# Performance work log

Hardware: AMD Instinct MI355X
Metric: run time of the kernel (lower is better)

Reference implementation:

```python
import jax, jax.numpy as jnp
import numpy as np

N_HEADS = 8
EMBED_C = 256  # key/query channels
OUT_C = 256    # value/output channels
MASK_CENTER = True

def setup_inputs() -> dict:
    key = jax.random.key(0)
    ks = jax.random.split(key, 5)
    B, C, H, W = 32, 256, 32, 32
    x = jax.random.normal(ks[0], (B, C, H, W), dtype=jnp.float32)
    # 1x1 conv weights as [out, in] matrices; scaled like torch conv default init
    s = 1.0 / np.sqrt(C)
    q_w = jax.random.normal(ks[1], (EMBED_C, C), dtype=jnp.float32) * s
    q_b = jax.random.normal(ks[2], (EMBED_C,), dtype=jnp.float32) * s
    kv_w = jax.random.normal(ks[3], (EMBED_C + OUT_C, C), dtype=jnp.float32) * s
    kv_b = jax.random.normal(ks[4], (EMBED_C + OUT_C,), dtype=jnp.float32) * s
    return {"x": x, "q_w": q_w, "q_b": q_b, "kv_w": kv_w, "kv_b": kv_b}

def _to_multihead(t):
    # t: (B, C, S) -> (B, n_heads, S, C // n_heads)
    B, C, S = t.shape
    return jnp.transpose(t.reshape(B, N_HEADS, C // N_HEADS, S), (0, 1, 3, 2))

def reference(x, q_w, q_b, kv_w, kv_b):
    B, C, H, W = x.shape
    S = H * W
    xf = x.reshape(B, C, S)  # flatten spatial; 1x1 conv == channel matmul
    q = jnp.einsum('oc,bcs->bos', q_w, xf) + q_b[None, :, None]
    kv = jnp.einsum('oc,bcs->bos', kv_w, xf) + kv_b[None, :, None]
    k, v = kv[:, :EMBED_C], kv[:, EMBED_C:]
    q = _to_multihead(q)   # (B, h, S, dk)
    k = _to_multihead(k)   # (B, h, S, dk)
    v = _to_multihead(v)   # (B, h, S, dv)
    dk = k.shape[-1]
    # strictly-lower-triangular causal mask (center pixel masked)
    mask = jnp.tril(jnp.ones((S, S), dtype=x.dtype), -int(MASK_CENTER))
    scores = jnp.einsum('bhqd,bhkd->bhqk', q, k) / jnp.sqrt(jnp.asarray(dk, x.dtype))
    scores = jnp.where(mask == 0, jnp.asarray(-10000.0, x.dtype), scores)
    attn = jax.nn.softmax(scores, axis=-1)
    attn = jnp.where(mask == 0, jnp.asarray(0.0, x.dtype), attn)
    out = jnp.einsum('bhqk,bhkd->bhqd', attn, v)  # (B, h, S, dv)
    out = jnp.transpose(out, (0, 1, 3, 2)).reshape(B, OUT_C, H, W)
    return out
```

## Files before the change

kernel.cpp:

```cpp
#include <hip/hip_runtime.h>
#include <hip/hip_bf16.h>

typedef __attribute__((ext_vector_type(8))) short short8;
typedef __attribute__((ext_vector_type(4))) float f32x4;
typedef __attribute__((ext_vector_type(16))) float f32x16;

#define B_  32
#define CH  256
#define S_  1024
#define NH  8
#define HD  32

static __device__ __forceinline__ unsigned short f2bf(float f) {
  __hip_bfloat16 h = __float2bfloat16(f);
  return *reinterpret_cast<unsigned short*>(&h);
}

static __device__ __forceinline__ void gl_lds16(const void* g, void* l) {
  __builtin_amdgcn_global_load_lds(
      (const __attribute__((address_space(1))) void*)g,
      (__attribute__((address_space(3))) void*)l, 16, 0, 0);
}

__global__ void k_prep(const float* __restrict__ x, unsigned short* __restrict__ xt,
                       const float* __restrict__ qw, const float* __restrict__ qb,
                       const float* __restrict__ kvw, const float* __restrict__ kvb,
                       unsigned short* __restrict__ wt, float* __restrict__ bias) {
  __shared__ float tile[32][33];
  int blk = (int)blockIdx.x;
  int t = threadIdx.x;
  if (blk < 8192) {
    int b = blk >> 8;
    int inner = blk & 255;
    int ct = inner >> 5, st = inner & 31;
    int c0 = ct * 32, s0 = st * 32;
    int r = t >> 3, q4 = (t & 7) * 4;
    const float4 v = *reinterpret_cast<const float4*>(
        x + ((size_t)(b * CH + c0 + r)) * S_ + s0 + q4);
    tile[r][q4 + 0] = v.x; tile[r][q4 + 1] = v.y;
    tile[r][q4 + 2] = v.z; tile[r][q4 + 3] = v.w;
    __syncthreads();
    ushort4 u;
    u.x = f2bf(tile[q4 + 0][r]); u.y = f2bf(tile[q4 + 1][r]);
    u.z = f2bf(tile[q4 + 2][r]); u.w = f2bf(tile[q4 + 3][r]);
    *reinterpret_cast<ushort4*>(xt + ((size_t)(b * S_ + s0 + r)) * CH + c0 + q4) = u;
  } else {
    int gid = (blk - 8192) * 256 + t;
    const float rs = 0.25503531838951954f;
    int o = gid >> 8, c = gid & 255;
    float v = (o < 256) ? qw[o * 256 + c] * rs : kvw[(o - 256) * 256 + c];
    wt[gid] = f2bf(v);
    if (gid < 768) bias[gid] = (gid < 256) ? qb[gid] * rs : kvb[gid - 256];
  }
}

__global__ __launch_bounds__(256) void k_proj(
    const unsigned short* __restrict__ wt, const float* __restrict__ bias,
    const unsigned short* __restrict__ xt,
    unsigned short* __restrict__ qws, unsigned short* __restrict__ kv) {
  __shared__ __align__(16) unsigned short As[2][4096];
  __shared__ __align__(16) unsigned short Bs[2][4096];
  int b = blockIdx.y;
  int mt = blockIdx.x >> 3, nt = blockIdx.x & 7;
  int tid = threadIdx.x;
  int wid = tid >> 6, l = tid & 63;
  int rb = l >> 4, lr = l & 15;
  int wr = wid >> 1, wc = wid & 1;
  int mb = mt * 128, nb = nt * 128;
  int wm = wr * 64, wn = wc * 64;
  const unsigned short* xb = xt + (size_t)b * S_ * CH;

  int r0 = tid >> 2, k0 = (tid & 3) * 8;
  int r1 = (tid + 256) >> 2, k1 = ((tid + 256) & 3) * 8;
  const unsigned short* wa0 = wt + (size_t)(mb + r0) * CH + k0;
  const unsigned short* wa1 = wt + (size_t)(mb + r1) * CH + k1;
  const unsigned short* xb0 = xb + (size_t)(nb + r0) * CH + k0;
  const unsigned short* xb1 = xb + (size_t)(nb + r1) * CH + k1;
  char* asb = (char*)&As[0][0];
  char* bsb = (char*)&Bs[0][0];
  int wb = wid * 1024;

  f32x4 acc[4][4];
  #pragma unroll
  for (int mf = 0; mf < 4; ++mf)
    #pragma unroll
    for (int nf = 0; nf < 4; ++nf)
      acc[mf][nf] = (f32x4){0.f, 0.f, 0.f, 0.f};

  gl_lds16(wa0, asb + wb);
  gl_lds16(wa1, asb + 4096 + wb);
  gl_lds16(xb0, bsb + wb);
  gl_lds16(xb1, bsb + 4096 + wb);
  __syncthreads();

  #pragma unroll 1
  for (int kk = 0; kk < 8; ++kk) {
    int cur = kk & 1;
    bool more = (kk < 7);
    if (more) {
      int ko = (kk + 1) * 32;
      int bo = (cur ^ 1) * 8192 + wb;
      gl_lds16(wa0 + ko, asb + bo);
      gl_lds16(wa1 + ko, asb + 4096 + bo);
      gl_lds16(xb0 + ko, bsb + bo);
      gl_lds16(xb1 + ko, bsb + 4096 + bo);
    }

    short8 a[4], bfr[4];
    #pragma unroll
    for (int mf = 0; mf < 4; ++mf)
      a[mf] = *reinterpret_cast<const short8*>(
          &As[cur][(wm + mf * 16 + lr) * 32 + rb * 8]);
    #pragma unroll
    for (int nf = 0; nf < 4; ++nf)
      bfr[nf] = *reinterpret_cast<const short8*>(
          &Bs[cur][(wn + nf * 16 + lr) * 32 + rb * 8]);
    #pragma unroll
    for (int mf = 0; mf < 4; ++mf)
      #pragma unroll
      for (int nf = 0; nf < 4; ++nf)
        acc[mf][nf] = __builtin_amdgcn_mfma_f32_16x16x32_bf16(
            a[mf], bfr[nf], acc[mf][nf], 0, 0, 0);

    __syncthreads();
  }

  #pragma unroll
  for (int mf = 0; mf < 4; ++mf) {
    int m0 = mb + wm + mf * 16 + rb * 4;
    const float4 bv = *reinterpret_cast<const float4*>(bias + m0);
    #pragma unroll
    for (int nf = 0; nf < 4; ++nf) {
      int n = nb + wn + nf * 16 + lr;
      float v0 = acc[mf][nf][0] + bv.x;
      float v1 = acc[mf][nf][1] + bv.y;
      float v2 = acc[mf][nf][2] + bv.z;
      float v3 = acc[mf][nf][3] + bv.w;
      if (m0 < 256) {
        int h = m0 >> 5, d = m0 & 31;
        ushort4 u = {f2bf(v0), f2bf(v1), f2bf(v2), f2bf(v3)};
        *reinterpret_cast<ushort4*>(
            qws + ((size_t)(b * NH + h) * S_ + n) * HD + d) = u;
      } else if (m0 < 512) {
        int mm = m0 - 256; int h = mm >> 5, d0 = mm & 31;
        size_t off = (((size_t)(b * NH + h) * 32 + (n >> 5)) * 2048)
                   + (size_t)((d0 >> 3) * 256 + (n & 31) * 8 + (d0 & 7));
        ushort4 u = {f2bf(v0), f2bf(v1), f2bf(v2), f2bf(v3)};
        *reinterpret_cast<ushort4*>(kv + off) = u;
      } else {
        int mm = m0 - 512; int h = mm >> 5, d0 = mm & 31;
        int nl = n & 31;
        int kp = (nl & 19) | (((nl >> 2) & 1) << 3) | (((nl >> 3) & 1) << 2);
        size_t base = (((size_t)(b * NH + h) * 32 + (n >> 5)) * 2048) + 1024
                    + (size_t)((kp >> 3) * 256 + (kp & 7));
        kv[base + (size_t)(d0 + 0) * 8] = f2bf(v0);
        kv[base + (size_t)(d0 + 1) * 8] = f2bf(v1);
        kv[base + (size_t)(d0 + 2) * 8] = f2bf(v2);
        kv[base + (size_t)(d0 + 3) * 8] = f2bf(v3);
      }
    }
  }
}

__global__ __launch_bounds__(512, 4) void k_attn(
    const unsigned short* __restrict__ qws, const unsigned short* __restrict__ kv,
    float* __restrict__ out) {
  __shared__ __align__(16) unsigned short kvbuf[2][8192];
  int tid = threadIdx.x;
  int wid = tid >> 6, l = tid & 63;
  int col = l & 31, hi = l >> 5;
  int bh = (int)(blockIdx.x & 255);
  int g  = 3 - (int)(blockIdx.x >> 8);
  int qt = g * 8 + wid;
  int q0 = qt << 5;
  int niter = g * 2 + 2;

  const unsigned short* Q   = qws + (size_t)bh * S_ * HD;
  const unsigned short* kvb = kv + (size_t)bh * 32 * 2048;
  char* kb0 = (char*)&kvbuf[0][0];
  int wb = wid * 1024;

  short8 aq0 = *reinterpret_cast<const short8*>(Q + (q0 + col) * HD + hi * 8);
  short8 aq1 = *reinterpret_cast<const short8*>(Q + (q0 + col) * HD + 16 + hi * 8);

  f32x16 z, O;
  #pragma unroll
  for (int i = 0; i < 16; ++i) { z[i] = 0.f; O[i] = 0.f; }
  float lsA = 0.f, lsB = 0.f;

  gl_lds16(kvb + tid * 8,        kb0 + wb);
  gl_lds16(kvb + 4096 + tid * 8, kb0 + 8192 + wb);
  __syncthreads();

  #pragma unroll 1
  for (int i = 0; i < niter; ++i) {
    int cur = i & 1;
    bool more = (i + 1 < niter);
    if (more) {
      const unsigned short* src = kvb + (size_t)(i + 1) * 8192 + tid * 8;
      char* dst = kb0 + (cur ^ 1) * 16384 + wb;
      gl_lds16(src,        dst);
      gl_lds16(src + 4096, dst + 8192);
    }

    #pragma unroll
    for (int sub = 0; sub < 4; ++sub) {
      int t = 4 * i + sub;
      if (qt >= t) {
        const unsigned short* Kb = &kvbuf[cur][sub * 2048];
        short8 bk0 = *reinterpret_cast<const short8*>(Kb + hi * 256 + col * 8);
        short8 bk1 = *reinterpret_cast<const short8*>(Kb + 512 + hi * 256 + col * 8);
        short8 av0 = *reinterpret_cast<const short8*>(Kb + 1024 + hi * 256 + col * 8);
        short8 av1 = *reinterpret_cast<const short8*>(Kb + 1536 + hi * 256 + col * 8);

        f32x16 st = __builtin_amdgcn_mfma_f32_32x32x16_bf16(bk0, aq0, z, 0, 0, 0);
        st = __builtin_amdgcn_mfma_f32_32x32x16_bf16(bk1, aq1, st, 0, 0, 0);

        float p[16];
        if (t == qt) {
          #pragma unroll
          for (int r = 0; r < 16; ++r) {
            int key = (r & 3) + 8 * (r >> 2) + 4 * hi;
            float e = __builtin_amdgcn_exp2f(st[r]);
            p[r] = (key < col) ? e : 0.f;
          }
        } else {
          #pragma unroll
          for (int r = 0; r < 16; ++r) p[r] = __builtin_amdgcn_exp2f(st[r]);
        }

        lsA += ((p[0] + p[1]) + (p[2] + p[3])) + ((p[4] + p[5]) + (p[6] + p[7]));
        lsB += ((p[8] + p[9]) + (p[10] + p[11])) + ((p[12] + p[13]) + (p[14] + p[15]));

        union { unsigned int u[8]; short8 v[2]; } pb;
        #pragma unroll
        for (int jj = 0; jj < 8; ++jj)
          asm("v_cvt_pk_bf16_f32 %0, %1, %2"
              : "=v"(pb.u[jj]) : "v"(p[2 * jj]), "v"(p[2 * jj + 1]));

        O = __builtin_amdgcn_mfma_f32_32x32x16_bf16(av0, pb.v[0], O, 0, 0, 0);
        O = __builtin_amdgcn_mfma_f32_32x32x16_bf16(av1, pb.v[1], O, 0, 0, 0);
      }
    }

    __syncthreads();
  }

  float lsum = lsA + lsB;
  float ltot = lsum + __shfl_xor(lsum, 32);
  float linv = (ltot > 0.f) ? 1.f / ltot : 0.f;
  int b = bh >> 3, h = bh & 7;
  float* ob = out + ((size_t)(b * 256 + h * 32)) * S_ + q0 + col;
  #pragma unroll
  for (int r = 0; r < 16; ++r) {
    int d = (r & 3) + 8 * (r >> 2) + 4 * hi;
    ob[(size_t)d * S_] = O[r] * linv;
  }
}

extern "C" void kernel_launch(void* const* d_in, const int* in_sizes, int n_in,
                              void* d_out, int out_size, void* d_ws, size_t ws_size,
                              hipStream_t stream) {
  const float* x   = (const float*)d_in[0];
  const float* qw  = (const float*)d_in[1];
  const float* qb  = (const float*)d_in[2];
  const float* kvw = (const float*)d_in[3];
  const float* kvb = (const float*)d_in[4];
  float* out = (float*)d_out;

  char* ws = (char*)d_ws;
  unsigned short* wt   = (unsigned short*)(ws + 0);
  float*          bias = (float*)(ws + 393216);
  unsigned short* xt   = (unsigned short*)(ws + 396288);
  unsigned short* qws  = (unsigned short*)(ws + 17173504);
  unsigned short* kv   = (unsigned short*)(ws + 33950720);

  k_prep<<<8960, 256, 0, stream>>>(x, xt, qw, qb, kvw, kvb, wt, bias);
  k_proj<<<dim3(48, 32), 256, 0, stream>>>(wt, bias, xt, qws, kv);
  k_attn<<<1024, 512, 0, stream>>>(qws, kv, out);
}
```

Measured before the change: 73.43 us.

## Triple-buffer projection GEMM loads with manual vmcnt waits and k-major LDS layout

Replaces the double-buffered K loop in the QKV projection kernel with a fully unrolled three-stage pipeline. Two tiles are kept in flight, and each step waits with explicit s_waitcnt vmcnt and raw s_barrier instead of __syncthreads. The LDS tile layout also changes to k-chunk-major, so each row's 8-element slice sits contiguously per chunk, which alters the bank access pattern for MFMA fragment reads. The aim is to hide global-to-LDS latency better, at the cost of 50% more shared memory and reliance on hand-managed waits being correct.

```diff
diff --git a/kernel.cpp b/kernel.cpp
--- a/kernel.cpp
+++ b/kernel.cpp
@@ -54,12 +54,41 @@
   }
 }
 
+
+#define VMW(n) asm volatile("s_waitcnt vmcnt(" #n ")" ::: "memory")
+#define BARX() asm volatile("s_barrier" ::: "memory")
+
+#define PROJ_ISSUE(step, buf) do {                                  \
+    gl_lds16(wa + (step) * 32,      asb + (buf) * 8192 + wb);       \
+    gl_lds16(wa + (step) * 32 + 16, asb + (buf) * 8192 + 4096 + wb);\
+    gl_lds16(xa + (step) * 32,      bsb + (buf) * 8192 + wb);       \
+    gl_lds16(xa + (step) * 32 + 16, bsb + (buf) * 8192 + 4096 + wb);\
+  } while (0)
+
+#define PROJ_COMPUTE(buf) do {                                      \
+    short8 af[4], bfv[4];                                           \
+    _Pragma("unroll")                                               \
+    for (int mf = 0; mf < 4; ++mf)                                  \
+      af[mf] = *reinterpret_cast<const short8*>(                    \
+          &As[buf][rb * 1024 + (wm + mf * 16 + lr) * 8]);           \
+    _Pragma("unroll")                                               \
+    for (int nf = 0; nf < 4; ++nf)                                  \
+      bfv[nf] = *reinterpret_cast<const short8*>(                   \
+          &Bs[buf][rb * 1024 + (wn + nf * 16 + lr) * 8]);           \
+    _Pragma("unroll")                                               \
+    for (int mf = 0; mf < 4; ++mf)                                  \
+      _Pragma("unroll")                                             \
+      for (int nf = 0; nf < 4; ++nf)                                \
+        acc[mf][nf] = __builtin_amdgcn_mfma_f32_16x16x32_bf16(      \
+            af[mf], bfv[nf], acc[mf][nf], 0, 0, 0);                 \
+  } while (0)
+
 __global__ __launch_bounds__(256) void k_proj(
     const unsigned short* __restrict__ wt, const float* __restrict__ bias,
     const unsigned short* __restrict__ xt,
     unsigned short* __restrict__ qws, unsigned short* __restrict__ kv) {
-  __shared__ __align__(16) unsigned short As[2][4096];
-  __shared__ __align__(16) unsigned short Bs[2][4096];
+  __shared__ __align__(16) unsigned short As[3][4096];
+  __shared__ __align__(16) unsigned short Bs[3][4096];
   int b = blockIdx.y;
   int mt = blockIdx.x >> 3, nt = blockIdx.x & 7;
   int tid = threadIdx.x;
@@ -70,12 +99,9 @@
   int wm = wr * 64, wn = wc * 64;
   const unsigned short* xb = xt + (size_t)b * S_ * CH;
 
-  int r0 = tid >> 2, k0 = (tid & 3) * 8;
-  int r1 = (tid + 256) >> 2, k1 = ((tid + 256) & 3) * 8;
-  const unsigned short* wa0 = wt + (size_t)(mb + r0) * CH + k0;
-  const unsigned short* wa1 = wt + (size_t)(mb + r1) * CH + k1;
-  const unsigned short* xb0 = xb + (size_t)(nb + r0) * CH + k0;
-  const unsigned short* xb1 = xb + (size_t)(nb + r1) * CH + k1;
+  int rrow = tid & 127, kb2 = tid >> 7;
+  const unsigned short* wa = wt + (size_t)(mb + rrow) * CH + kb2 * 8;
+  const unsigned short* xa = xb + (size_t)(nb + rrow) * CH + kb2 * 8;
   char* asb = (char*)&As[0][0];
   char* bsb = (char*)&Bs[0][0];
   int wb = wid * 1024;
@@ -87,43 +113,16 @@
     for (int nf = 0; nf < 4; ++nf)
       acc[mf][nf] = (f32x4){0.f, 0.f, 0.f, 0.f};
 
-  gl_lds16(wa0, asb + wb);
-  gl_lds16(wa1, asb + 4096 + wb);
-  gl_lds16(xb0, bsb + wb);
-  gl_lds16(xb1, bsb + 4096 + wb);
-  __syncthreads();
-
-  #pragma unroll 1
-  for (int kk = 0; kk < 8; ++kk) {
-    int cur = kk & 1;
-    bool more = (kk < 7);
-    if (more) {
-      int ko = (kk + 1) * 32;
-      int bo = (cur ^ 1) * 8192 + wb;
-      gl_lds16(wa0 + ko, asb + bo);
-      gl_lds16(wa1 + ko, asb + 4096 + bo);
-      gl_lds16(xb0 + ko, bsb + bo);
-      gl_lds16(xb1 + ko, bsb + 4096 + bo);
-    }
-
-    short8 a[4], bfr[4];
-    #pragma unroll
-    for (int mf = 0; mf < 4; ++mf)
-      a[mf] = *reinterpret_cast<const short8*>(
-          &As[cur][(wm + mf * 16 + lr) * 32 + rb * 8]);
-    #pragma unroll
-    for (int nf = 0; nf < 4; ++nf)
-      bfr[nf] = *reinterpret_cast<const short8*>(
-          &Bs[cur][(wn + nf * 16 + lr) * 32 + rb * 8]);
-    #pragma unroll
-    for (int mf = 0; mf < 4; ++mf)
-      #pragma unroll
-      for (int nf = 0; nf < 4; ++nf)
-        acc[mf][nf] = __builtin_amdgcn_mfma_f32_16x16x32_bf16(
-            a[mf], bfr[nf], acc[mf][nf], 0, 0, 0);
-
-    __syncthreads();
-  }
+  PROJ_ISSUE(0, 0); PROJ_ISSUE(1, 1);
+
+  VMW(4); BARX(); PROJ_ISSUE(2, 2); PROJ_COMPUTE(0);
+  VMW(4); BARX(); PROJ_ISSUE(3, 0); PROJ_COMPUTE(1);
+  VMW(4); BARX(); PROJ_ISSUE(4, 1); PROJ_COMPUTE(2);
+  VMW(4); BARX(); PROJ_ISSUE(5, 2); PROJ_COMPUTE(0);
+  VMW(4); BARX(); PROJ_ISSUE(6, 0); PROJ_COMPUTE(1);
+  VMW(4); BARX(); PROJ_ISSUE(7, 1); PROJ_COMPUTE(2);
+  VMW(4); BARX();                   PROJ_COMPUTE(0);
+  VMW(0); BARX();                   PROJ_COMPUTE(1);
 
   #pragma unroll
   for (int mf = 0; mf < 4; ++mf) {
```

New measurement: 79.81 us. +8.7%, slower.
